# Kernel tuning notes

Measured on AMD Instinct MI355X. Metric: run time of the kernel, lower is better.

## Reference

```python
import jax, jax.numpy as jnp
import numpy as np

HEAD_DIM = 128
N_HEADS = 32
N_KV_HEADS = 8
N_REP = N_HEADS // N_KV_HEADS


def _rope(t, cos, sin):
    # t: [b, s, h, d]; cos/sin: [s, d//2]; rotate interleaved pairs (complex mult)
    b, s, h, d = t.shape
    t = t.reshape(b, s, h, d // 2, 2)
    t0, t1 = t[..., 0], t[..., 1]
    c = cos[None, :, None, :]
    sn = sin[None, :, None, :]
    r0 = t0 * c - t1 * sn
    r1 = t0 * sn + t1 * c
    return jnp.stack([r0, r1], axis=-1).reshape(b, s, h, d)


def setup_inputs() -> dict:
    key = jax.random.key(0)
    ks = jax.random.split(key, 6)
    b, s, dim = 2, 2048, 4096
    x = jax.random.normal(ks[0], (b, s, dim), dtype=jnp.float32)
    wq = jax.random.normal(ks[1], (N_HEADS * HEAD_DIM, dim), dtype=jnp.float32) * 0.02
    wk = jax.random.normal(ks[2], (N_KV_HEADS * HEAD_DIM, dim), dtype=jnp.float32) * 0.02
    wv = jax.random.normal(ks[3], (N_KV_HEADS * HEAD_DIM, dim), dtype=jnp.float32) * 0.02
    wo = jax.random.normal(ks[4], (dim, N_HEADS * HEAD_DIM), dtype=jnp.float32) * 0.02
    # precompute_freqs_cis: theta = 10000, freqs over half head_dim
    inv = 1.0 / (10000.0 ** (np.arange(0, HEAD_DIM, 2)[: HEAD_DIM // 2] / HEAD_DIM))
    ang = np.outer(np.arange(s), inv).astype(np.float32)  # [s, d//2]
    freqs_cos = jnp.asarray(np.cos(ang))
    freqs_sin = jnp.asarray(np.sin(ang))
    # causal additive mask
    mask = jnp.triu(jnp.full((s, s), -jnp.inf, dtype=jnp.float32), k=1)
    return {"x": x, "wq": wq, "wk": wk, "wv": wv, "wo": wo,
            "freqs_cos": freqs_cos, "freqs_sin": freqs_sin, "mask": mask,
            "start_pos": 0}


def reference(x, wq, wk, wv, wo, freqs_cos, freqs_sin, mask, start_pos):
    b, s, dim = x.shape
    xq = (x @ wq.T).reshape(b, s, N_HEADS, HEAD_DIM)
    xk = (x @ wk.T).reshape(b, s, N_KV_HEADS, HEAD_DIM)
    xv = (x @ wv.T).reshape(b, s, N_KV_HEADS, HEAD_DIM)
    xq = _rope(xq, freqs_cos, freqs_sin)
    xk = _rope(xk, freqs_cos, freqs_sin)
    # full prefill (start_pos=0): keys/values == current xk/xv
    # GQA via broadcast instead of materialized repeat_kv (same math)
    q = xq.transpose(0, 2, 1, 3).reshape(b, N_KV_HEADS, N_REP, s, HEAD_DIM)
    k = xk.transpose(0, 2, 1, 3)  # [b, kvh, s, d]
    v = xv.transpose(0, 2, 1, 3)
    scores = jnp.einsum('bgnqd,bgkd->bgnqk', q, k) / jnp.sqrt(
        jnp.asarray(HEAD_DIM, dtype=x.dtype))
    scores = scores + mask[None, None, None, :, :]
    probs = jax.nn.softmax(scores.astype(jnp.float32), axis=-1).astype(x.dtype)
    out = jnp.einsum('bgnqk,bgkd->bgnqd', probs, v)  # [b, kvh, n_rep, s, d]
    out = out.reshape(b, N_HEADS, s, HEAD_DIM).transpose(0, 2, 1, 3).reshape(b, s, -1)
    return out @ wo.T
```

## Files before the change

### kernel.cpp

```cpp
#include <hip/hip_runtime.h>
#include <hip/hip_fp16.h>
#include <stdint.h>
#include <stddef.h>

typedef _Float16 f16;
typedef __attribute__((ext_vector_type(4))) _Float16 f16x4;
typedef __attribute__((ext_vector_type(8))) _Float16 f16x8;
typedef __attribute__((ext_vector_type(4))) float f32x4;
typedef __attribute__((ext_vector_type(16))) float f32x16;

__device__ __forceinline__ void gld_lds16(const void* g, void* l) {
  __builtin_amdgcn_global_load_lds((const __attribute__((address_space(1))) void*)g,
                                   (__attribute__((address_space(3))) void*)l, 16, 0, 0);
}

__global__ void cast_all(const float* __restrict__ x, const float* __restrict__ wq,
                         const float* __restrict__ wk, const float* __restrict__ wv,
                         const float* __restrict__ wo, f16* __restrict__ xh,
                         f16* __restrict__ wqh, f16* __restrict__ wkh,
                         f16* __restrict__ wvh, f16* __restrict__ woh) {
  int i = blockIdx.x * blockDim.x + threadIdx.x;
  const float* in;
  f16* out;
  int j = i;
  if (j < 4194304) { in = x; out = xh; }
  else if ((j -= 4194304) < 4194304) { in = wq; out = wqh; }
  else if ((j -= 4194304) < 1048576) { in = wk; out = wkh; }
  else if ((j -= 1048576) < 1048576) { in = wv; out = wvh; }
  else { j -= 1048576; in = wo; out = woh; }
  float4 v = ((const float4*)in)[j];
  f16x4 h;
  h[0] = (f16)v.x; h[1] = (f16)v.y; h[2] = (f16)v.z; h[3] = (f16)v.w;
  *(f16x4*)(out + (size_t)j * 4) = h;
}

__device__ __forceinline__ void gemm_core_4096(const f16* __restrict__ Ab,
                                               const f16* __restrict__ Bb,
                                               f16* As, f16* Bs, f32x16 acc[2][2]) {
  const int tid = threadIdx.x, ln = tid & 63, wv = tid >> 6;
  const int wr = wv >> 1, wc = wv & 1;
  const int l31 = ln & 31, half = ln >> 5;
#pragma unroll
  for (int a = 0; a < 2; ++a)
#pragma unroll
    for (int b = 0; b < 2; ++b)
#pragma unroll
      for (int r = 0; r < 16; ++r) acc[a][b][r] = 0.f;

  int srow[2], scol[2];
#pragma unroll
  for (int c = 0; c < 2; ++c) {
    int chunk = wv * 2 + c;
    int lineL = chunk * 8 + (ln >> 3);
    int s = (ln & 7) ^ (lineL & 7);
    srow[c] = lineL * 2 + (s >> 2);
    scol[c] = (s & 3) * 8;
  }
  const int rb = l31 >> 1;
  const int bxor = ((l31 & 1) * 4) ^ (rb & 7);

  for (int k0 = 0; k0 < 4096; k0 += 32) {
#pragma unroll
    for (int c = 0; c < 2; ++c) {
      int chunk = wv * 2 + c;
      gld_lds16(Ab + (size_t)srow[c] * 4096 + k0 + scol[c], As + chunk * 512);
      gld_lds16(Bb + (size_t)srow[c] * 4096 + k0 + scol[c], Bs + chunk * 512);
    }
    __syncthreads();
    f16x8 af[2][2], bf[2][2];
#pragma unroll
    for (int tm = 0; tm < 2; ++tm) {
      int lbase = (wr * 32 + tm * 16 + rb) * 64;
#pragma unroll
      for (int ks = 0; ks < 2; ++ks)
        af[tm][ks] = *(const f16x8*)&As[lbase + (((ks * 2 + half) ^ bxor) * 8)];
    }
#pragma unroll
    for (int tn = 0; tn < 2; ++tn) {
      int lbase = (wc * 32 + tn * 16 + rb) * 64;
#pragma unroll
      for (int ks = 0; ks < 2; ++ks)
        bf[tn][ks] = *(const f16x8*)&Bs[lbase + (((ks * 2 + half) ^ bxor) * 8)];
    }
#pragma unroll
    for (int tm = 0; tm < 2; ++tm)
#pragma unroll
      for (int tn = 0; tn < 2; ++tn) {
        acc[tm][tn] = __builtin_amdgcn_mfma_f32_32x32x16_f16(af[tm][0], bf[tn][0], acc[tm][tn], 0, 0, 0);
        acc[tm][tn] = __builtin_amdgcn_mfma_f32_32x32x16_f16(af[tm][1], bf[tn][1], acc[tm][tn], 0, 0, 0);
      }
    __syncthreads();
  }
}

__global__ __launch_bounds__(256, 4) void gemm_qkv(
    const f16* __restrict__ xh, const f16* __restrict__ wqh,
    const f16* __restrict__ wkh, const f16* __restrict__ wvh,
    f16* __restrict__ qh, f16* __restrict__ kh, f16* __restrict__ vt) {
  __shared__ __align__(16) f16 As[4096];
  __shared__ __align__(16) f16 Bs[4096];
  const int bx = blockIdx.x, by = blockIdx.y;
  const f16* Bb;
  if (bx < 32)      Bb = wqh + (size_t)bx * 128 * 4096;
  else if (bx < 40) Bb = wkh + (size_t)(bx - 32) * 128 * 4096;
  else              Bb = wvh + (size_t)(bx - 40) * 128 * 4096;
  f32x16 acc[2][2];
  gemm_core_4096(xh + (size_t)by * 128 * 4096, Bb, As, Bs, acc);
  const int tid = threadIdx.x, ln = tid & 63, wv = tid >> 6;
  const int wr = wv >> 1, wc = wv & 1;
  const int l31 = ln & 31, half = ln >> 5;
#pragma unroll
  for (int tm = 0; tm < 2; ++tm)
#pragma unroll
    for (int tn = 0; tn < 2; ++tn) {
      int colb = wc * 64 + tn * 32 + l31;
#pragma unroll
      for (int g = 0; g < 4; ++g) {
        int mb = by * 128 + wr * 64 + tm * 32 + g * 8 + half * 4;
        if (bx < 32) {
#pragma unroll
          for (int r2 = 0; r2 < 4; ++r2)
            qh[(size_t)(mb + r2) * 4096 + bx * 128 + colb] = (f16)acc[tm][tn][g * 4 + r2];
        } else if (bx < 40) {
#pragma unroll
          for (int r2 = 0; r2 < 4; ++r2)
            kh[(size_t)(mb + r2) * 1024 + (bx - 32) * 128 + colb] = (f16)acc[tm][tn][g * 4 + r2];
        } else {
          f16x4 v4;
#pragma unroll
          for (int r2 = 0; r2 < 4; ++r2) v4[r2] = (f16)acc[tm][tn][g * 4 + r2];
          int n2 = (bx - 40) * 128 + colb;
          int kv = n2 >> 7, d = n2 & 127;
          int bbv = mb >> 11, sl = mb & 2047;
          *(f16x4*)&vt[(((size_t)bbv * 8 + kv) * 128 + d) * 2048 + sl] = v4;
        }
      }
    }
}

__global__ void rope_qk(f16* __restrict__ qh, f16* __restrict__ kh,
                        const float* __restrict__ fc, const float* __restrict__ fs) {
  int i = blockIdx.x * blockDim.x + threadIdx.x;
  const int QG = 4096 * 32 * 16;
  f16* ptr;
  int sl, p0;
  if (i < QG) {
    int g = i & 15, head = (i >> 4) & 31, tok = i >> 9;
    sl = tok & 2047; p0 = g * 4;
    ptr = qh + (size_t)tok * 4096 + head * 128 + g * 8;
  } else {
    int j = i - QG;
    int g = j & 15, head = (j >> 4) & 7, tok = j >> 7;
    sl = tok & 2047; p0 = g * 4;
    ptr = kh + (size_t)tok * 1024 + head * 128 + g * 8;
  }
  f16x8 v = *(f16x8*)ptr;
  float4 c = *(const float4*)&fc[sl * 64 + p0];
  float4 s = *(const float4*)&fs[sl * 64 + p0];
  f16x8 o;
  o[0] = (f16)((float)v[0] * c.x - (float)v[1] * s.x);
  o[1] = (f16)((float)v[0] * s.x + (float)v[1] * c.x);
  o[2] = (f16)((float)v[2] * c.y - (float)v[3] * s.y);
  o[3] = (f16)((float)v[2] * s.y + (float)v[3] * c.y);
  o[4] = (f16)((float)v[4] * c.z - (float)v[5] * s.z);
  o[5] = (f16)((float)v[4] * s.z + (float)v[5] * c.z);
  o[6] = (f16)((float)v[6] * c.w - (float)v[7] * s.w);
  o[7] = (f16)((float)v[6] * s.w + (float)v[7] * c.w);
  *(f16x8*)ptr = o;
}

__global__ __launch_bounds__(256, 4) void attn(
    const f16* __restrict__ qh, const f16* __restrict__ kh,
    const f16* __restrict__ vt, f16* __restrict__ ao) {
  __shared__ __align__(16) f16 Kl[64 * 128];
  __shared__ __align__(16) f16 Vl[128 * 64];
  __shared__ __align__(16) f16 Pl[4][16 * 64];
  const int qt = 31 - blockIdx.x;
  const int h = blockIdx.y, bb = blockIdx.z;
  const int kvh = h >> 2;
  const int tid = threadIdx.x, ln = tid & 63, wv = tid >> 6;
  const int quad = ln >> 4, c16 = ln & 15;

  f16x8 Qf[4];
  {
    size_t qbase = ((size_t)(bb * 2048 + qt * 64 + wv * 16 + c16)) * 4096 + h * 128;
#pragma unroll
    for (int ks = 0; ks < 4; ++ks)
      Qf[ks] = *(const f16x8*)&qh[qbase + ks * 32 + quad * 8];
  }
  float m_run = -INFINITY, l_run = 0.f;
  f32x4 Ot[8];
#pragma unroll
  for (int n = 0; n < 8; ++n) { f32x4 z = {0.f, 0.f, 0.f, 0.f}; Ot[n] = z; }
  const float scale = 0.08838834764831843f;
  const int qg = qt * 64 + wv * 16 + c16;
  const int swp = ((quad ^ (c16 & 7)) * 8);
  const int swp1 = (((4 + quad) ^ (c16 & 7)) * 8);

  for (int t = 0; t <= qt; ++t) {
#pragma unroll
    for (int c = 0; c < 4; ++c) {
      int chunk = wv * 4 + c;
      int krow = chunk * 4 + (ln >> 4);
      int kg = (ln & 15) ^ (krow & 15);
      gld_lds16(&kh[((size_t)(bb * 2048 + t * 64 + krow)) * 1024 + kvh * 128 + kg * 8],
                &Kl[chunk * 512]);
    }
#pragma unroll
    for (int c = 0; c < 4; ++c) {
      int chunk = wv * 4 + c;
      int vrow = chunk * 8 + (ln >> 3);
      int vg = (ln & 7) ^ (vrow & 7);
      gld_lds16(&vt[(((size_t)bb * 8 + kvh) * 128 + vrow) * 2048 + t * 64 + vg * 8],
                &Vl[chunk * 512]);
    }
    __syncthreads();

    f32x4 Sa[4];
#pragma unroll
    for (int tn = 0; tn < 4; ++tn) {
      f32x4 z = {0.f, 0.f, 0.f, 0.f};
      Sa[tn] = z;
#pragma unroll
      for (int ks = 0; ks < 4; ++ks) {
        f16x8 kf = *(const f16x8*)&Kl[(tn * 16 + c16) * 128 + (((ks * 4 + quad) ^ c16) * 8)];
        Sa[tn] = __builtin_amdgcn_mfma_f32_16x16x32_f16(kf, Qf[ks], Sa[tn], 0, 0, 0);
      }
    }

#pragma unroll
    for (int tn = 0; tn < 4; ++tn)
#pragma unroll
      for (int r = 0; r < 4; ++r) Sa[tn][r] *= scale;
    if (t == qt) {
#pragma unroll
      for (int tn = 0; tn < 4; ++tn) {
        int kbase = t * 64 + tn * 16 + quad * 4;
#pragma unroll
        for (int r = 0; r < 4; ++r)
          if (kbase + r > qg) Sa[tn][r] = -INFINITY;
      }
    }

    float mm = -INFINITY;
#pragma unroll
    for (int tn = 0; tn < 4; ++tn)
#pragma unroll
      for (int r = 0; r < 4; ++r) mm = fmaxf(mm, Sa[tn][r]);
    mm = fmaxf(mm, __shfl_xor(mm, 16, 64));
    mm = fmaxf(mm, __shfl_xor(mm, 32, 64));
    float mn = fmaxf(m_run, mm);
    float alpha = __expf(m_run - mn);
    m_run = mn;
    float rsum = 0.f;
#pragma unroll
    for (int tn = 0; tn < 4; ++tn)
#pragma unroll
      for (int r = 0; r < 4; ++r) {
        float p = __expf(Sa[tn][r] - mn);
        Sa[tn][r] = p;
        rsum += p;
      }
    rsum += __shfl_xor(rsum, 16, 64);
    rsum += __shfl_xor(rsum, 32, 64);
    l_run = l_run * alpha + rsum;

#pragma unroll
    for (int tn = 0; tn < 4; ++tn) {
      f16x4 pk;
#pragma unroll
      for (int r = 0; r < 4; ++r) pk[r] = (f16)Sa[tn][r];
      int g = tn * 2 + (quad >> 1);
      *(f16x4*)&Pl[wv][c16 * 64 + ((g ^ (c16 & 7)) * 8) + (quad & 1) * 4] = pk;
    }

#pragma unroll
    for (int n = 0; n < 8; ++n)
#pragma unroll
      for (int r = 0; r < 4; ++r) Ot[n][r] *= alpha;

    __asm__ volatile("s_waitcnt lgkmcnt(0)" ::: "memory");

    {
      f16x8 pf0 = *(const f16x8*)&Pl[wv][c16 * 64 + swp];
      f16x8 pf1 = *(const f16x8*)&Pl[wv][c16 * 64 + swp1];
#pragma unroll
      for (int n = 0; n < 8; ++n) {
        int rowv = (n * 16 + c16) * 64;
        f16x8 vf0 = *(const f16x8*)&Vl[rowv + swp];
        Ot[n] = __builtin_amdgcn_mfma_f32_16x16x32_f16(vf0, pf0, Ot[n], 0, 0, 0);
        f16x8 vf1 = *(const f16x8*)&Vl[rowv + swp1];
        Ot[n] = __builtin_amdgcn_mfma_f32_16x16x32_f16(vf1, pf1, Ot[n], 0, 0, 0);
      }
    }
    __syncthreads();
  }

  float inv = 1.0f / l_run;
  size_t token = (size_t)(bb * 2048 + qt * 64 + wv * 16 + c16);
#pragma unroll
  for (int n = 0; n < 8; ++n) {
    f16x4 o;
#pragma unroll
    for (int r = 0; r < 4; ++r) o[r] = (f16)(Ot[n][r] * inv);
    *(f16x4*)&ao[token * 4096 + h * 128 + n * 16 + quad * 4] = o;
  }
}

__global__ __launch_bounds__(256, 4) void gemm_out(
    const f16* __restrict__ ao, const f16* __restrict__ woh, float* __restrict__ out) {
  __shared__ __align__(16) f16 As[4096];
  __shared__ __align__(16) f16 Bs[4096];
  f32x16 acc[2][2];
  gemm_core_4096(ao + (size_t)blockIdx.y * 128 * 4096,
                 woh + (size_t)blockIdx.x * 128 * 4096, As, Bs, acc);
  const int tid = threadIdx.x, ln = tid & 63, wv = tid >> 6;
  const int wr = wv >> 1, wc = wv & 1;
  const int l31 = ln & 31, half = ln >> 5;
#pragma unroll
  for (int tm = 0; tm < 2; ++tm)
#pragma unroll
    for (int tn = 0; tn < 2; ++tn) {
      int n = blockIdx.x * 128 + wc * 64 + tn * 32 + l31;
#pragma unroll
      for (int g = 0; g < 4; ++g) {
        int mb = blockIdx.y * 128 + wr * 64 + tm * 32 + g * 8 + half * 4;
#pragma unroll
        for (int r2 = 0; r2 < 4; ++r2)
          out[(size_t)(mb + r2) * 4096 + n] = acc[tm][tn][g * 4 + r2];
      }
    }
}

extern "C" void kernel_launch(void* const* d_in, const int* in_sizes, int n_in,
                              void* d_out, int out_size, void* d_ws, size_t ws_size,
                              hipStream_t stream) {
  const float* x  = (const float*)d_in[0];
  const float* wq = (const float*)d_in[1];
  const float* wk = (const float*)d_in[2];
  const float* wv = (const float*)d_in[3];
  const float* wo = (const float*)d_in[4];
  const float* fc = (const float*)d_in[5];
  const float* fs = (const float*)d_in[6];
  float* out = (float*)d_out;

  char* ws = (char*)d_ws;
  f16* xh  = (f16*)(ws + 0);
  f16* wqh = (f16*)(ws + 33554432);
  f16* wkh = (f16*)(ws + 67108864);
  f16* wvh = (f16*)(ws + 75497472);
  f16* woh = (f16*)(ws + 83886080);
  f16* qh  = (f16*)(ws + 117440512);
  f16* kh  = (f16*)(ws + 150994944);
  f16* vt  = (f16*)(ws + 159383552);
  f16* ao  = (f16*)(ws + 167772160);

  cast_all<<<57344, 256, 0, stream>>>(x, wq, wk, wv, wo, xh, wqh, wkh, wvh, woh);
  gemm_qkv<<<dim3(48, 32), 256, 0, stream>>>(xh, wqh, wkh, wvh, qh, kh, vt);
  rope_qk<<<10240, 256, 0, stream>>>(qh, kh, fc, fs);
  attn<<<dim3(32, 32, 2), 256, 0, stream>>>(qh, kh, vt, ao);
  gemm_out<<<dim3(32, 32), 256, 0, stream>>>(ao, woh, out);
}
```

Measured before the change: 877.2 us.

## Rewrite projection GEMMs with 256x128 tiles and triple-buffered async LDS pipeline

Replaces the single-buffered 128x128 GEMM core with a 256x128 tile per 512-thread block. It triple-buffers K=64 slices in LDS via global_load_lds, using explicit vmcnt waits and raw barriers so loads overlap the MFMA work. It also switches to 16x16x32 MFMAs with 4x4 accumulators per wave, raises MFMA priority with setprio, and swizzles block ids for L2 locality. The aim is to hide global load latency and raise arithmetic intensity in the QKV and output projections, at the cost of larger LDS use and lower occupancy.

New measurement: 778.1 us. 11.3% less time.

```diff
diff --git a/kernel.cpp b/kernel.cpp
--- a/kernel.cpp
+++ b/kernel.cpp
@@ -7,11 +7,16 @@
 typedef __attribute__((ext_vector_type(4))) _Float16 f16x4;
 typedef __attribute__((ext_vector_type(8))) _Float16 f16x8;
 typedef __attribute__((ext_vector_type(4))) float f32x4;
-typedef __attribute__((ext_vector_type(16))) float f32x16;
 
 __device__ __forceinline__ void gld_lds16(const void* g, void* l) {
   __builtin_amdgcn_global_load_lds((const __attribute__((address_space(1))) void*)g,
                                    (__attribute__((address_space(3))) void*)l, 16, 0, 0);
+}
+
+template <int N>
+__device__ __forceinline__ void wait_vmcnt() {
+  if constexpr (N == 0) __asm__ volatile("s_waitcnt vmcnt(0)" ::: "memory");
+  else if constexpr (N == 6) __asm__ volatile("s_waitcnt vmcnt(6)" ::: "memory");
 }
 
 __global__ void cast_all(const float* __restrict__ x, const float* __restrict__ wq,
@@ -34,106 +39,149 @@
   *(f16x4*)(out + (size_t)j * 4) = h;
 }
 
-__device__ __forceinline__ void gemm_core_4096(const f16* __restrict__ Ab,
-                                               const f16* __restrict__ Bb,
-                                               f16* As, f16* Bs, f32x16 acc[2][2]) {
+__device__ __forceinline__ void gemm_core256(const f16* __restrict__ Ab,
+                                             const f16* __restrict__ Bb,
+                                             f16* __restrict__ lds,
+                                             f32x4 acc[4][4]) {
   const int tid = threadIdx.x, ln = tid & 63, wv = tid >> 6;
   const int wr = wv >> 1, wc = wv & 1;
-  const int l31 = ln & 31, half = ln >> 5;
-#pragma unroll
-  for (int a = 0; a < 2; ++a)
-#pragma unroll
-    for (int b = 0; b < 2; ++b)
-#pragma unroll
-      for (int r = 0; r < 16; ++r) acc[a][b][r] = 0.f;
-
-  int srow[2], scol[2];
-#pragma unroll
-  for (int c = 0; c < 2; ++c) {
-    int chunk = wv * 2 + c;
-    int lineL = chunk * 8 + (ln >> 3);
-    int s = (ln & 7) ^ (lineL & 7);
-    srow[c] = lineL * 2 + (s >> 2);
-    scol[c] = (s & 3) * 8;
-  }
-  const int rb = l31 >> 1;
-  const int bxor = ((l31 & 1) * 4) ^ (rb & 7);
-
-  for (int k0 = 0; k0 < 4096; k0 += 32) {
-#pragma unroll
-    for (int c = 0; c < 2; ++c) {
-      int chunk = wv * 2 + c;
-      gld_lds16(Ab + (size_t)srow[c] * 4096 + k0 + scol[c], As + chunk * 512);
-      gld_lds16(Bb + (size_t)srow[c] * 4096 + k0 + scol[c], Bs + chunk * 512);
-    }
-    __syncthreads();
-    f16x8 af[2][2], bf[2][2];
-#pragma unroll
-    for (int tm = 0; tm < 2; ++tm) {
-      int lbase = (wr * 32 + tm * 16 + rb) * 64;
-#pragma unroll
-      for (int ks = 0; ks < 2; ++ks)
-        af[tm][ks] = *(const f16x8*)&As[lbase + (((ks * 2 + half) ^ bxor) * 8)];
-    }
-#pragma unroll
-    for (int tn = 0; tn < 2; ++tn) {
-      int lbase = (wc * 32 + tn * 16 + rb) * 64;
-#pragma unroll
-      for (int ks = 0; ks < 2; ++ks)
-        bf[tn][ks] = *(const f16x8*)&Bs[lbase + (((ks * 2 + half) ^ bxor) * 8)];
-    }
-#pragma unroll
-    for (int tm = 0; tm < 2; ++tm)
-#pragma unroll
-      for (int tn = 0; tn < 2; ++tn) {
-        acc[tm][tn] = __builtin_amdgcn_mfma_f32_32x32x16_f16(af[tm][0], bf[tn][0], acc[tm][tn], 0, 0, 0);
-        acc[tm][tn] = __builtin_amdgcn_mfma_f32_32x32x16_f16(af[tm][1], bf[tn][1], acc[tm][tn], 0, 0, 0);
-      }
-    __syncthreads();
-  }
-}
-
-__global__ __launch_bounds__(256, 4) void gemm_qkv(
+  const int c16 = ln & 15, quad = ln >> 4;
+#pragma unroll
+  for (int mi = 0; mi < 4; ++mi)
+#pragma unroll
+    for (int ni = 0; ni < 4; ++ni) {
+      f32x4 z = {0.f, 0.f, 0.f, 0.f};
+      acc[mi][ni] = z;
+    }
+  int srA[4], scA[4];
+#pragma unroll
+  for (int u = 0; u < 4; ++u) {
+    int P = u * 512 + wv * 64 + ln;
+    int pr = P >> 3;
+    srA[u] = pr;
+    scA[u] = ((P & 7) ^ (pr & 7)) * 8;
+  }
+  int offA[4], offB[4];
+#pragma unroll
+  for (int i = 0; i < 4; ++i) {
+    offA[i] = (wr * 64 + i * 16 + c16) * 64;
+    offB[i] = (wc * 64 + i * 16 + c16) * 64;
+  }
+  const int gk0 = ((0 + quad) ^ (c16 & 7)) * 8;
+  const int gk1 = ((4 + quad) ^ (c16 & 7)) * 8;
+
+#define STAGE(BUF, K0)                                                        \
+  {                                                                           \
+    _Pragma("unroll") for (int u = 0; u < 4; ++u) {                           \
+      gld_lds16(Ab + (size_t)srA[u] * 4096 + (K0) + scA[u],                   \
+                lds + (BUF) + (u * 512 + wv * 64) * 8);                       \
+    }                                                                         \
+    _Pragma("unroll") for (int u = 0; u < 2; ++u) {                           \
+      gld_lds16(Bb + (size_t)srA[u] * 4096 + (K0) + scA[u],                   \
+                lds + (BUF) + 16384 + (u * 512 + wv * 64) * 8);               \
+    }                                                                         \
+  }
+
+#define READS(BUF, GK)                                                        \
+  _Pragma("unroll") for (int i = 0; i < 4; ++i) {                             \
+    af[i] = *(const f16x8*)&lds[(BUF) + offA[i] + (GK)];                      \
+  }                                                                           \
+  _Pragma("unroll") for (int i = 0; i < 4; ++i) {                             \
+    bf[i] = *(const f16x8*)&lds[(BUF) + 16384 + offB[i] + (GK)];              \
+  }
+
+#define BARRIER()                                                             \
+  __builtin_amdgcn_sched_barrier(0);                                          \
+  __builtin_amdgcn_s_barrier();                                               \
+  __builtin_amdgcn_sched_barrier(0);
+
+#define MFMA16()                                                              \
+  __builtin_amdgcn_s_setprio(1);                                              \
+  _Pragma("unroll") for (int mi = 0; mi < 4; ++mi) {                          \
+    _Pragma("unroll") for (int ni = 0; ni < 4; ++ni) {                        \
+      acc[mi][ni] = __builtin_amdgcn_mfma_f32_16x16x32_f16(                   \
+          af[mi], bf[ni], acc[mi][ni], 0, 0, 0);                              \
+    }                                                                         \
+  }                                                                           \
+  __builtin_amdgcn_s_setprio(0);
+
+  int b0 = 0, b1 = 24576, b2 = 49152;
+  f16x8 af[4], bf[4];
+
+  STAGE(b0, 0);
+  STAGE(b1, 64);
+  wait_vmcnt<6>();
+  BARRIER();
+
+#pragma unroll 1
+  for (int t = 0; t < 62; ++t) {
+    READS(b0, gk0);
+    BARRIER();
+    MFMA16();
+    READS(b0, gk1);
+    STAGE(b2, (t + 2) * 64);
+    wait_vmcnt<6>();
+    BARRIER();
+    MFMA16();
+    int tmp = b0; b0 = b1; b1 = b2; b2 = tmp;
+  }
+  READS(b0, gk0);
+  BARRIER();
+  MFMA16();
+  READS(b0, gk1);
+  wait_vmcnt<0>();
+  BARRIER();
+  MFMA16();
+  READS(b1, gk0);
+  MFMA16();
+  READS(b1, gk1);
+  MFMA16();
+
+#undef STAGE
+#undef READS
+#undef BARRIER
+#undef MFMA16
+}
+
+__global__ __launch_bounds__(512, 2) void gemm_qkv(
     const f16* __restrict__ xh, const f16* __restrict__ wqh,
     const f16* __restrict__ wkh, const f16* __restrict__ wvh,
     f16* __restrict__ qh, f16* __restrict__ kh, f16* __restrict__ vt) {
-  __shared__ __align__(16) f16 As[4096];
-  __shared__ __align__(16) f16 Bs[4096];
-  const int bx = blockIdx.x, by = blockIdx.y;
+  __shared__ __align__(16) f16 lds[73728];
+  const int id = blockIdx.x;
+  const int swz = (id & 7) * 96 + (id >> 3);
+  const int bx = swz % 48, by = swz / 48;
   const f16* Bb;
   if (bx < 32)      Bb = wqh + (size_t)bx * 128 * 4096;
   else if (bx < 40) Bb = wkh + (size_t)(bx - 32) * 128 * 4096;
   else              Bb = wvh + (size_t)(bx - 40) * 128 * 4096;
-  f32x16 acc[2][2];
-  gemm_core_4096(xh + (size_t)by * 128 * 4096, Bb, As, Bs, acc);
+  f32x4 acc[4][4];
+  gemm_core256(xh + (size_t)by * 256 * 4096, Bb, lds, acc);
   const int tid = threadIdx.x, ln = tid & 63, wv = tid >> 6;
   const int wr = wv >> 1, wc = wv & 1;
-  const int l31 = ln & 31, half = ln >> 5;
-#pragma unroll
-  for (int tm = 0; tm < 2; ++tm)
-#pragma unroll
-    for (int tn = 0; tn < 2; ++tn) {
-      int colb = wc * 64 + tn * 32 + l31;
-#pragma unroll
-      for (int g = 0; g < 4; ++g) {
-        int mb = by * 128 + wr * 64 + tm * 32 + g * 8 + half * 4;
-        if (bx < 32) {
-#pragma unroll
-          for (int r2 = 0; r2 < 4; ++r2)
-            qh[(size_t)(mb + r2) * 4096 + bx * 128 + colb] = (f16)acc[tm][tn][g * 4 + r2];
-        } else if (bx < 40) {
-#pragma unroll
-          for (int r2 = 0; r2 < 4; ++r2)
-            kh[(size_t)(mb + r2) * 1024 + (bx - 32) * 128 + colb] = (f16)acc[tm][tn][g * 4 + r2];
-        } else {
-          f16x4 v4;
-#pragma unroll
-          for (int r2 = 0; r2 < 4; ++r2) v4[r2] = (f16)acc[tm][tn][g * 4 + r2];
-          int n2 = (bx - 40) * 128 + colb;
-          int kv = n2 >> 7, d = n2 & 127;
-          int bbv = mb >> 11, sl = mb & 2047;
-          *(f16x4*)&vt[(((size_t)bbv * 8 + kv) * 128 + d) * 2048 + sl] = v4;
-        }
+  const int c16 = ln & 15, quad = ln >> 4;
+#pragma unroll
+  for (int mi = 0; mi < 4; ++mi)
+#pragma unroll
+    for (int ni = 0; ni < 4; ++ni) {
+      int colb = wc * 64 + ni * 16 + c16;
+      int m0 = by * 256 + wr * 64 + mi * 16 + quad * 4;
+      if (bx < 32) {
+#pragma unroll
+        for (int r = 0; r < 4; ++r)
+          qh[(size_t)(m0 + r) * 4096 + bx * 128 + colb] = (f16)acc[mi][ni][r];
+      } else if (bx < 40) {
+#pragma unroll
+        for (int r = 0; r < 4; ++r)
+          kh[(size_t)(m0 + r) * 1024 + (bx - 32) * 128 + colb] = (f16)acc[mi][ni][r];
+      } else {
+        f16x4 v4;
+#pragma unroll
+        for (int r = 0; r < 4; ++r) v4[r] = (f16)acc[mi][ni][r];
+        int n2 = (bx - 40) * 128 + colb;
+        int kv = n2 >> 7, d = n2 & 127;
+        int bbv = m0 >> 11, sl = m0 & 2047;
+        *(f16x4*)&vt[(((size_t)bbv * 8 + kv) * 128 + d) * 2048 + sl] = v4;
       }
     }
 }
@@ -307,28 +355,26 @@
   }
 }
 
-__global__ __launch_bounds__(256, 4) void gemm_out(
+__global__ __launch_bounds__(512, 2) void gemm_out(
     const f16* __restrict__ ao, const f16* __restrict__ woh, float* __restrict__ out) {
-  __shared__ __align__(16) f16 As[4096];
-  __shared__ __align__(16) f16 Bs[4096];
-  f32x16 acc[2][2];
-  gemm_core_4096(ao + (size_t)blockIdx.y * 128 * 4096,
-                 woh + (size_t)blockIdx.x * 128 * 4096, As, Bs, acc);
+  __shared__ __align__(16) f16 lds[73728];
+  const int id = blockIdx.x;
+  const int swz = (id & 7) * 64 + (id >> 3);
+  const int bx = swz % 32, by = swz / 32;
+  f32x4 acc[4][4];
+  gemm_core256(ao + (size_t)by * 256 * 4096, woh + (size_t)bx * 128 * 4096, lds, acc);
   const int tid = threadIdx.x, ln = tid & 63, wv = tid >> 6;
   const int wr = wv >> 1, wc = wv & 1;
-  const int l31 = ln & 31, half = ln >> 5;
-#pragma unroll
-  for (int tm = 0; tm < 2; ++tm)
-#pragma unroll
-    for (int tn = 0; tn < 2; ++tn) {
-      int n = blockIdx.x * 128 + wc * 64 + tn * 32 + l31;
-#pragma unroll
-      for (int g = 0; g < 4; ++g) {
-        int mb = blockIdx.y * 128 + wr * 64 + tm * 32 + g * 8 + half * 4;
-#pragma unroll
-        for (int r2 = 0; r2 < 4; ++r2)
-          out[(size_t)(mb + r2) * 4096 + n] = acc[tm][tn][g * 4 + r2];
-      }
+  const int c16 = ln & 15, quad = ln >> 4;
+#pragma unroll
+  for (int mi = 0; mi < 4; ++mi)
+#pragma unroll
+    for (int ni = 0; ni < 4; ++ni) {
+      int n = bx * 128 + wc * 64 + ni * 16 + c16;
+      int m0 = by * 256 + wr * 64 + mi * 16 + quad * 4;
+#pragma unroll
+      for (int r = 0; r < 4; ++r)
+        out[(size_t)(m0 + r) * 4096 + n] = acc[mi][ni][r];
     }
 }
 
@@ -356,8 +402,8 @@
   f16* ao  = (f16*)(ws + 167772160);
 
   cast_all<<<57344, 256, 0, stream>>>(x, wq, wk, wv, wo, xh, wqh, wkh, wvh, woh);
-  gemm_qkv<<<dim3(48, 32), 256, 0, stream>>>(xh, wqh, wkh, wvh, qh, kh, vt);
+  gemm_qkv<<<768, 512, 0, stream>>>(xh, wqh, wkh, wvh, qh, kh, vt);
   rope_qk<<<10240, 256, 0, stream>>>(qh, kh, fc, fs);
   attn<<<dim3(32, 32, 2), 256, 0, stream>>>(qh, kh, vt, ao);
-  gemm_out<<<dim3(32, 32), 256, 0, stream>>>(ao, woh, out);
-}
+  gemm_out<<<512, 512, 0, stream>>>(ao, woh, out);
+}
```

## Rework projection GEMMs with large double-buffered LDS tiles and block swizzle

Applied to the files above, without the earlier changes.

Replaces the 128x128, K=32, single-buffered GEMM core with a templated core using 256x256 (out) or 256x384 (QKV) tiles. It runs 512 threads, takes K steps of 64, and double-buffers LDS so the next tile's global-to-LDS load overlaps MFMA work. The QKV GEMM now treats the contiguous wq/wk/wv half-precision buffers as one concatenated weight matrix. Both GEMMs launch 256 blocks with an XCD-aware block-id swizzle. The aim is more operand reuse per LDS load and less barrier stall, at the cost of very high LDS use per block (about 160KB for QKV), which allows only one block per CU and a single wave of blocks.

Result: faster. 794.4 us (-9.4%).

```diff
diff --git a/kernel.cpp b/kernel.cpp
--- a/kernel.cpp
+++ b/kernel.cpp
@@ -12,6 +12,10 @@
 __device__ __forceinline__ void gld_lds16(const void* g, void* l) {
   __builtin_amdgcn_global_load_lds((const __attribute__((address_space(1))) void*)g,
                                    (__attribute__((address_space(3))) void*)l, 16, 0, 0);
+}
+
+__device__ __forceinline__ void vm0() {
+  __asm__ volatile("s_waitcnt vmcnt(0)" ::: "memory");
 }
 
 __global__ void cast_all(const float* __restrict__ x, const float* __restrict__ wq,
@@ -34,104 +38,132 @@
   *(f16x4*)(out + (size_t)j * 4) = h;
 }
 
-__device__ __forceinline__ void gemm_core_4096(const f16* __restrict__ Ab,
-                                               const f16* __restrict__ Bb,
-                                               f16* As, f16* Bs, f32x16 acc[2][2]) {
+template <int NF>
+__device__ __forceinline__ void gemm_core(const f16* __restrict__ Ab,
+                                          const f16* __restrict__ Bb,
+                                          f16* __restrict__ lds,
+                                          f32x16 acc[4][NF]) {
+  constexpr int BN = NF * 128;
+  constexpr int S = 16384 + BN * 64;
+  constexpr int BU = BN / 64;
   const int tid = threadIdx.x, ln = tid & 63, wv = tid >> 6;
-  const int wr = wv >> 1, wc = wv & 1;
-  const int l31 = ln & 31, half = ln >> 5;
-#pragma unroll
-  for (int a = 0; a < 2; ++a)
-#pragma unroll
-    for (int b = 0; b < 2; ++b)
-#pragma unroll
-      for (int r = 0; r < 16; ++r) acc[a][b][r] = 0.f;
-
-  int srow[2], scol[2];
-#pragma unroll
-  for (int c = 0; c < 2; ++c) {
-    int chunk = wv * 2 + c;
-    int lineL = chunk * 8 + (ln >> 3);
-    int s = (ln & 7) ^ (lineL & 7);
-    srow[c] = lineL * 2 + (s >> 2);
-    scol[c] = (s & 3) * 8;
-  }
-  const int rb = l31 >> 1;
-  const int bxor = ((l31 & 1) * 4) ^ (rb & 7);
-
-  for (int k0 = 0; k0 < 4096; k0 += 32) {
-#pragma unroll
-    for (int c = 0; c < 2; ++c) {
-      int chunk = wv * 2 + c;
-      gld_lds16(Ab + (size_t)srow[c] * 4096 + k0 + scol[c], As + chunk * 512);
-      gld_lds16(Bb + (size_t)srow[c] * 4096 + k0 + scol[c], Bs + chunk * 512);
-    }
-    __syncthreads();
-    f16x8 af[2][2], bf[2][2];
-#pragma unroll
-    for (int tm = 0; tm < 2; ++tm) {
-      int lbase = (wr * 32 + tm * 16 + rb) * 64;
-#pragma unroll
-      for (int ks = 0; ks < 2; ++ks)
-        af[tm][ks] = *(const f16x8*)&As[lbase + (((ks * 2 + half) ^ bxor) * 8)];
-    }
-#pragma unroll
-    for (int tn = 0; tn < 2; ++tn) {
-      int lbase = (wc * 32 + tn * 16 + rb) * 64;
-#pragma unroll
-      for (int ks = 0; ks < 2; ++ks)
-        bf[tn][ks] = *(const f16x8*)&Bs[lbase + (((ks * 2 + half) ^ bxor) * 8)];
-    }
-#pragma unroll
-    for (int tm = 0; tm < 2; ++tm)
-#pragma unroll
-      for (int tn = 0; tn < 2; ++tn) {
-        acc[tm][tn] = __builtin_amdgcn_mfma_f32_32x32x16_f16(af[tm][0], bf[tn][0], acc[tm][tn], 0, 0, 0);
-        acc[tm][tn] = __builtin_amdgcn_mfma_f32_32x32x16_f16(af[tm][1], bf[tn][1], acc[tm][tn], 0, 0, 0);
-      }
-    __syncthreads();
-  }
-}
-
-__global__ __launch_bounds__(256, 4) void gemm_qkv(
-    const f16* __restrict__ xh, const f16* __restrict__ wqh,
-    const f16* __restrict__ wkh, const f16* __restrict__ wvh,
+  const int wr = wv >> 2, wc = wv & 3;
+  const int l31 = ln & 31, h32 = ln >> 5;
+  const int x7 = l31 & 7;
+#pragma unroll
+  for (int mi = 0; mi < 4; ++mi)
+#pragma unroll
+    for (int ni = 0; ni < NF; ++ni)
+#pragma unroll
+      for (int r = 0; r < 16; ++r) acc[mi][ni][r] = 0.f;
+
+  int sA[4], sB[BU];
+#pragma unroll
+  for (int u = 0; u < 4; ++u) {
+    int P = u * 512 + tid;
+    sA[u] = (P >> 3) * 4096 + (((P & 7) ^ ((P >> 3) & 7)) * 8);
+  }
+#pragma unroll
+  for (int u = 0; u < BU; ++u) {
+    int P = u * 512 + tid;
+    sB[u] = (P >> 3) * 4096 + (((P & 7) ^ ((P >> 3) & 7)) * 8);
+  }
+  int rA[4], rB[NF];
+#pragma unroll
+  for (int mi = 0; mi < 4; ++mi) rA[mi] = (wr * 128 + mi * 32 + l31) * 64;
+#pragma unroll
+  for (int ni = 0; ni < NF; ++ni) rB[ni] = 16384 + (wc * (NF * 32) + ni * 32 + l31) * 64;
+
+#define STAGE(BUF, K0)                                                        \
+  {                                                                           \
+    _Pragma("unroll") for (int u = 0; u < 4; ++u) {                           \
+      gld_lds16(Ab + sA[u] + (K0), lds + (BUF) + (u * 512 + wv * 64) * 8);    \
+    }                                                                         \
+    _Pragma("unroll") for (int u = 0; u < BU; ++u) {                          \
+      gld_lds16(Bb + sB[u] + (K0),                                            \
+                lds + (BUF) + 16384 + (u * 512 + wv * 64) * 8);               \
+    }                                                                         \
+  }
+
+#define TILE_COMPUTE(BUF)                                                     \
+  _Pragma("unroll") for (int ks = 0; ks < 4; ++ks) {                          \
+    f16x8 af[4];                                                              \
+    f16x8 bf[NF];                                                             \
+    int gk = ((ks * 2 + h32) ^ x7) * 8;                                       \
+    _Pragma("unroll") for (int mi = 0; mi < 4; ++mi) {                        \
+      af[mi] = *(const f16x8*)&lds[(BUF) + rA[mi] + gk];                      \
+    }                                                                         \
+    _Pragma("unroll") for (int ni = 0; ni < NF; ++ni) {                       \
+      bf[ni] = *(const f16x8*)&lds[(BUF) + rB[ni] + gk];                      \
+    }                                                                         \
+    __builtin_amdgcn_s_setprio(1);                                            \
+    _Pragma("unroll") for (int mi = 0; mi < 4; ++mi) {                        \
+      _Pragma("unroll") for (int ni = 0; ni < NF; ++ni) {                     \
+        acc[mi][ni] = __builtin_amdgcn_mfma_f32_32x32x16_f16(                 \
+            af[mi], bf[ni], acc[mi][ni], 0, 0, 0);                            \
+      }                                                                       \
+    }                                                                         \
+    __builtin_amdgcn_s_setprio(0);                                            \
+  }
+
+#define SYNC()                                                                \
+  __builtin_amdgcn_sched_barrier(0);                                          \
+  vm0();                                                                      \
+  __builtin_amdgcn_s_barrier();                                               \
+  __builtin_amdgcn_sched_barrier(0);
+
+  int cur = 0, nxt = S;
+  STAGE(cur, 0);
+  SYNC();
+#pragma unroll 1
+  for (int t = 0; t < 63; ++t) {
+    STAGE(nxt, (t + 1) * 64);
+    TILE_COMPUTE(cur);
+    SYNC();
+    int tmp = cur; cur = nxt; nxt = tmp;
+  }
+  TILE_COMPUTE(cur);
+
+#undef STAGE
+#undef TILE_COMPUTE
+#undef SYNC
+}
+
+__global__ __launch_bounds__(512, 2) void gemm_qkv(
+    const f16* __restrict__ xh, const f16* __restrict__ wcat,
     f16* __restrict__ qh, f16* __restrict__ kh, f16* __restrict__ vt) {
-  __shared__ __align__(16) f16 As[4096];
-  __shared__ __align__(16) f16 Bs[4096];
-  const int bx = blockIdx.x, by = blockIdx.y;
-  const f16* Bb;
-  if (bx < 32)      Bb = wqh + (size_t)bx * 128 * 4096;
-  else if (bx < 40) Bb = wkh + (size_t)(bx - 32) * 128 * 4096;
-  else              Bb = wvh + (size_t)(bx - 40) * 128 * 4096;
-  f32x16 acc[2][2];
-  gemm_core_4096(xh + (size_t)by * 128 * 4096, Bb, As, Bs, acc);
+  __shared__ __align__(16) f16 lds[81920];
+  const int id = blockIdx.x;
+  const int swz = (id & 7) * 32 + (id >> 3);
+  const int bx = swz & 15, by = swz >> 4;
+  f32x16 acc[4][3];
+  gemm_core<3>(xh + (size_t)by * 256 * 4096, wcat + (size_t)bx * 384 * 4096, lds, acc);
   const int tid = threadIdx.x, ln = tid & 63, wv = tid >> 6;
-  const int wr = wv >> 1, wc = wv & 1;
-  const int l31 = ln & 31, half = ln >> 5;
-#pragma unroll
-  for (int tm = 0; tm < 2; ++tm)
-#pragma unroll
-    for (int tn = 0; tn < 2; ++tn) {
-      int colb = wc * 64 + tn * 32 + l31;
+  const int wr = wv >> 2, wc = wv & 3;
+  const int l31 = ln & 31, h32 = ln >> 5;
+#pragma unroll
+  for (int mi = 0; mi < 4; ++mi)
+#pragma unroll
+    for (int ni = 0; ni < 3; ++ni) {
+      int gc = bx * 384 + wc * 96 + ni * 32;
 #pragma unroll
       for (int g = 0; g < 4; ++g) {
-        int mb = by * 128 + wr * 64 + tm * 32 + g * 8 + half * 4;
-        if (bx < 32) {
+        int row = by * 256 + wr * 128 + mi * 32 + h32 * 4 + g * 8;
+        if (gc < 4096) {
 #pragma unroll
           for (int r2 = 0; r2 < 4; ++r2)
-            qh[(size_t)(mb + r2) * 4096 + bx * 128 + colb] = (f16)acc[tm][tn][g * 4 + r2];
-        } else if (bx < 40) {
+            qh[(size_t)(row + r2) * 4096 + gc + l31] = (f16)acc[mi][ni][g * 4 + r2];
+        } else if (gc < 5120) {
 #pragma unroll
           for (int r2 = 0; r2 < 4; ++r2)
-            kh[(size_t)(mb + r2) * 1024 + (bx - 32) * 128 + colb] = (f16)acc[tm][tn][g * 4 + r2];
+            kh[(size_t)(row + r2) * 1024 + (gc - 4096) + l31] = (f16)acc[mi][ni][g * 4 + r2];
         } else {
           f16x4 v4;
 #pragma unroll
-          for (int r2 = 0; r2 < 4; ++r2) v4[r2] = (f16)acc[tm][tn][g * 4 + r2];
-          int n2 = (bx - 40) * 128 + colb;
-          int kv = n2 >> 7, d = n2 & 127;
-          int bbv = mb >> 11, sl = mb & 2047;
+          for (int r2 = 0; r2 < 4; ++r2) v4[r2] = (f16)acc[mi][ni][g * 4 + r2];
+          int vcol = gc + l31 - 5120;
+          int kv = vcol >> 7, d = vcol & 127;
+          int bbv = row >> 11, sl = row & 2047;
           *(f16x4*)&vt[(((size_t)bbv * 8 + kv) * 128 + d) * 2048 + sl] = v4;
         }
       }
@@ -307,27 +339,28 @@
   }
 }
 
-__global__ __launch_bounds__(256, 4) void gemm_out(
+__global__ __launch_bounds__(512, 2) void gemm_out(
     const f16* __restrict__ ao, const f16* __restrict__ woh, float* __restrict__ out) {
-  __shared__ __align__(16) f16 As[4096];
-  __shared__ __align__(16) f16 Bs[4096];
-  f32x16 acc[2][2];
-  gemm_core_4096(ao + (size_t)blockIdx.y * 128 * 4096,
-                 woh + (size_t)blockIdx.x * 128 * 4096, As, Bs, acc);
+  __shared__ __align__(16) f16 lds[65536];
+  const int id = blockIdx.x;
+  const int swz = (id & 7) * 32 + (id >> 3);
+  const int bx = swz & 15, by = swz >> 4;
+  f32x16 acc[4][2];
+  gemm_core<2>(ao + (size_t)by * 256 * 4096, woh + (size_t)bx * 256 * 4096, lds, acc);
   const int tid = threadIdx.x, ln = tid & 63, wv = tid >> 6;
-  const int wr = wv >> 1, wc = wv & 1;
-  const int l31 = ln & 31, half = ln >> 5;
-#pragma unroll
-  for (int tm = 0; tm < 2; ++tm)
-#pragma unroll
-    for (int tn = 0; tn < 2; ++tn) {
-      int n = blockIdx.x * 128 + wc * 64 + tn * 32 + l31;
+  const int wr = wv >> 2, wc = wv & 3;
+  const int l31 = ln & 31, h32 = ln >> 5;
+#pragma unroll
+  for (int mi = 0; mi < 4; ++mi)
+#pragma unroll
+    for (int ni = 0; ni < 2; ++ni) {
+      int col = bx * 256 + wc * 64 + ni * 32 + l31;
 #pragma unroll
       for (int g = 0; g < 4; ++g) {
-        int mb = blockIdx.y * 128 + wr * 64 + tm * 32 + g * 8 + half * 4;
+        int row = by * 256 + wr * 128 + mi * 32 + h32 * 4 + g * 8;
 #pragma unroll
         for (int r2 = 0; r2 < 4; ++r2)
-          out[(size_t)(mb + r2) * 4096 + n] = acc[tm][tn][g * 4 + r2];
+          out[(size_t)(row + r2) * 4096 + col] = acc[mi][ni][g * 4 + r2];
       }
     }
 }
@@ -356,8 +389,8 @@
   f16* ao  = (f16*)(ws + 167772160);
 
   cast_all<<<57344, 256, 0, stream>>>(x, wq, wk, wv, wo, xh, wqh, wkh, wvh, woh);
-  gemm_qkv<<<dim3(48, 32), 256, 0, stream>>>(xh, wqh, wkh, wvh, qh, kh, vt);
+  gemm_qkv<<<256, 512, 0, stream>>>(xh, wqh, qh, kh, vt);
   rope_qk<<<10240, 256, 0, stream>>>(qh, kh, fc, fs);
   attn<<<dim3(32, 32, 2), 256, 0, stream>>>(qh, kh, vt, ao);
-  gemm_out<<<dim3(32, 32), 256, 0, stream>>>(ao, woh, out);
-}
+  gemm_out<<<256, 512, 0, stream>>>(ao, woh, out);
+}
```
